# Kernel tuning notes

Measured on AMD Instinct MI355X. Metric: run time of the kernel, lower is better.

## Reference

```python
import jax, jax.numpy as jnp
import numpy as np

B, C, H, W, N = 256, 64, 36, 36, 2000
P = H * W  # 1296 mask pixels


def setup_inputs() -> dict:
    key = jax.random.key(0)
    k1, k2, k3 = jax.random.split(key, 3)
    x = jax.random.normal(k1, (B, C, H, W), dtype=jnp.float32)
    # init_scales rows 1 and 2 give (mean=0, std=0.01) for both param tensors
    mask_weights = 0.01 * jax.random.normal(k2, (P, C, N), dtype=jnp.float32)
    readout_weights = 0.01 * jax.random.normal(k3, (C, N), dtype=jnp.float32)
    return {"x": x, "mask_weights": mask_weights, "readout_weights": readout_weights}


def reference(x, mask_weights, readout_weights):
    # x: (B, C, H, W) -> flatten spatial dims to P
    b, c, h, w = x.shape
    x_flat = x.reshape(b, c, h * w)  # (B, C, P)
    # Per-channel spatial pooling fused with weighted channel sum:
    # masked[b,c,n] = sum_p x_flat[b,c,p] * mask_weights[p,c,n]
    # out[b,n]     = sum_c masked[b,c,n] * readout_weights[c,n]
    out = jnp.einsum("bcp,pcn,cn->bn", x_flat, mask_weights, readout_weights)
    # final_relu=False => no bias / softplus
    return out
```

## Files before the change

kernel.cpp:

```cpp
#include <hip/hip_runtime.h>

typedef unsigned short ushort_t;
typedef unsigned int uint_t;
typedef __attribute__((ext_vector_type(8))) short bf16x8;
typedef __attribute__((ext_vector_type(4))) float f32x4;

#define C_DIM 64
#define P_DIM 1296
#define N_DIM 2000
#define B_DIM 256
#define K_DIM (C_DIM * P_DIM)
#define XB_ELEMS (B_DIM * K_DIM)
#define XB_ELEMS_PAD (XB_ELEMS + 256)
#define XB_BYTES ((size_t)XB_ELEMS_PAD * 2)
#define SLICES 32
#define OUT_ELEMS (B_DIM * N_DIM)
#define NSTEP 82

static __device__ __forceinline__ ushort_t f2bf(float f) {
  unsigned u = __builtin_bit_cast(unsigned, f);
  u += 0x7fffu + ((u >> 16) & 1u);
  return (ushort_t)(u >> 16);
}

__global__ void klindt_cvt_kernel(const float4* __restrict__ x,
                                  unsigned long long* __restrict__ xb) {
  int idx = blockIdx.x * 256 + threadIdx.x;
  if (idx >= XB_ELEMS_PAD / 4) return;
  unsigned long long r = 0ull;
  if (idx < XB_ELEMS / 4) {
    float4 v = x[idx];
    r = (unsigned long long)f2bf(v.x) | ((unsigned long long)f2bf(v.y) << 16) |
        ((unsigned long long)f2bf(v.z) << 32) |
        ((unsigned long long)f2bf(v.w) << 48);
  }
  xb[idx] = r;
}

__global__ void __launch_bounds__(512, 4) klindt_gemm_kernel(
    const char* __restrict__ xbb, const char* __restrict__ mwb,
    const float* __restrict__ rw, float* __restrict__ partials) {
  __shared__ ushort_t sA[3][8192];

  const int tid = threadIdx.x;
  const int lane = tid & 63;
  const int wid = tid >> 6;
  const int r15 = lane & 15, g4 = lane >> 4;
  const int bid = blockIdx.x;
  const int slice = (bid & 7) + 8 * ((bid >> 3) & 3);
  const int n0 = (bid >> 5) * 128;
  const int c0 = slice * 2;

  f32x4 acc[16];
#pragma unroll
  for (int i = 0; i < 16; ++i) {
    acc[i][0] = 0.f; acc[i][1] = 0.f; acc[i][2] = 0.f; acc[i][3] = 0.f;
  }

  uint_t a_gbase[2]; int a_doff[2];
#pragma unroll
  for (int it = 0; it < 2; ++it) {
    int chunk = it * 512 + tid;
    int row = chunk >> 2, t4 = chunk & 3;
    int ss = t4 ^ ((row >> 1) & 3);
    a_gbase[it] = (uint_t)(row * K_DIM + ss * 8) * 2u;
    a_doff[it] = chunk * 8;
  }

  const int nidx = n0 + wid * 16 + r15;
  const bool okn = nidx < N_DIM;
  const uint_t nb4 = (uint_t)(okn ? nidx : (N_DIM - 1)) * 4u;
  const float rvl = okn ? rw[c0 * N_DIM + nidx] : 0.f;
  const float rvh = okn ? rw[(c0 + 1) * N_DIM + nidx] : 0.f;
  const uint_t pg = (uint_t)(g4 * 8);

  const int swz = g4 ^ ((r15 >> 1) & 3);
  const int aoffbase = r15 * 32 + swz * 8;

  float mv[8];
  bf16x8 bfr;

  auto issueA = [&](int buf, int t) {
    int half = (t >= 41) ? 1 : 0;
    int sp = t - 41 * half;
    uint_t kb = ((uint_t)(c0 + half) * (uint_t)P_DIM + (uint_t)sp * 32u) * 2u;
#pragma unroll
    for (int it = 0; it < 2; ++it) {
      const char* g = xbb + (a_gbase[it] + kb);
      __builtin_amdgcn_global_load_lds(
          (const __attribute__((address_space(1))) unsigned int*)g,
          (__attribute__((address_space(3))) unsigned int*)(&sA[buf][a_doff[it]]),
          16, 0, 0);
    }
  };
  auto issueB = [&](int t) {
    int half = (t >= 41) ? 1 : 0;
    int sp = t - 41 * half;
    uint_t p0 = (uint_t)sp * 32u + pg;
    if (p0 > 1288u) p0 = 1288u;
    const char* bp = mwb + (p0 * 512000u + (uint_t)(c0 + half) * 8000u + nb4);
#pragma unroll
    for (int j = 0; j < 8; ++j)
      mv[j] = *(const float*)(bp + (uint_t)j * 512000u);
  };
  auto cvtB = [&](int t) {
    float rv = (t >= 41) ? rvh : rvl;
    if ((t == 40 || t == 81) && g4 >= 2) rv = 0.f;
#pragma unroll
    for (int j = 0; j < 8; ++j) bfr[j] = (short)f2bf(mv[j] * rv);
  };
  auto computeStep = [&](int buf) {
    __builtin_amdgcn_s_setprio(1);
#pragma unroll
    for (int fm = 0; fm < 16; ++fm) {
      bf16x8 afr = *(const bf16x8*)(&sA[buf][aoffbase + fm * 512]);
      acc[fm] = __builtin_amdgcn_mfma_f32_16x16x32_bf16(afr, bfr, acc[fm],
                                                        0, 0, 0);
    }
    __builtin_amdgcn_s_setprio(0);
  };

  issueB(0);
  issueA(0, 0);
  issueA(1, 1);
  asm volatile("s_waitcnt vmcnt(2) lgkmcnt(0)" ::: "memory");
  __builtin_amdgcn_sched_barrier(0);
  __builtin_amdgcn_s_barrier();
  __builtin_amdgcn_sched_barrier(0);

  int cur = 0;
  for (int s = 0; s < 80; ++s) {
    int bufW = (cur >= 1) ? cur - 1 : 2;
    cvtB(s);
    issueB(s + 1);
    issueA(bufW, s + 2);
    computeStep(cur);
    asm volatile("s_waitcnt vmcnt(10) lgkmcnt(0)" ::: "memory");
    __builtin_amdgcn_sched_barrier(0);
    __builtin_amdgcn_s_barrier();
    __builtin_amdgcn_sched_barrier(0);
    cur = (cur == 2) ? 0 : cur + 1;
  }
  cvtB(80);
  issueB(81);
  computeStep(2);
  asm volatile("s_waitcnt vmcnt(8) lgkmcnt(0)" ::: "memory");
  __builtin_amdgcn_sched_barrier(0);
  __builtin_amdgcn_s_barrier();
  __builtin_amdgcn_sched_barrier(0);
  cvtB(81);
  computeStep(0);

  float* pb = partials + (size_t)slice * OUT_ELEMS;
  if (okn) {
#pragma unroll
    for (int fm = 0; fm < 16; ++fm) {
#pragma unroll
      for (int rr = 0; rr < 4; ++rr) {
        int m = fm * 16 + g4 * 4 + rr;
        pb[m * N_DIM + nidx] = acc[fm][rr];
      }
    }
  }
}

__global__ void klindt_reduce_kernel(const float* __restrict__ part,
                                     float* __restrict__ out) {
  int i = blockIdx.x * 256 + threadIdx.x;
  if (i < OUT_ELEMS) {
    float s = 0.f;
#pragma unroll
    for (int k = 0; k < SLICES; ++k) s += part[(size_t)k * OUT_ELEMS + i];
    out[i] = s;
  }
}

extern "C" void kernel_launch(void* const* d_in, const int* in_sizes, int n_in,
                              void* d_out, int out_size, void* d_ws,
                              size_t ws_size, hipStream_t stream) {
  (void)in_sizes; (void)n_in; (void)out_size; (void)ws_size;
  const float* x = (const float*)d_in[0];
  const char* mwb = (const char*)d_in[1];
  const float* rw = (const float*)d_in[2];
  float* out = (float*)d_out;

  char* xbb = (char*)d_ws;
  float* partials = (float*)((char*)d_ws + XB_BYTES);

  {
    int nvec = XB_ELEMS_PAD / 4;
    int grid = (nvec + 255) / 256;
    klindt_cvt_kernel<<<grid, 256, 0, stream>>>((const float4*)x,
                                                (unsigned long long*)xbb);
  }
  {
    klindt_gemm_kernel<<<512, 512, 0, stream>>>(xbb, mwb, rw, partials);
  }
  {
    int grid = (OUT_ELEMS + 255) / 256;
    klindt_reduce_kernel<<<grid, 256, 0, stream>>>(partials, out);
  }
}
```

Baseline: 247.9 us.

## Double K-step size to 64 with double-buffered LDS and ping-pong B registers

```diff
diff --git a/kernel.cpp b/kernel.cpp
--- a/kernel.cpp
+++ b/kernel.cpp
@@ -15,7 +15,7 @@
 #define XB_BYTES ((size_t)XB_ELEMS_PAD * 2)
 #define SLICES 32
 #define OUT_ELEMS (B_DIM * N_DIM)
-#define NSTEP 82
+#define NSTEP 42
 
 static __device__ __forceinline__ ushort_t f2bf(float f) {
   unsigned u = __builtin_bit_cast(unsigned, f);
@@ -40,7 +40,7 @@
 __global__ void __launch_bounds__(512, 4) klindt_gemm_kernel(
     const char* __restrict__ xbb, const char* __restrict__ mwb,
     const float* __restrict__ rw, float* __restrict__ partials) {
-  __shared__ ushort_t sA[3][8192];
+  __shared__ ushort_t sA[2][16384];
 
   const int tid = threadIdx.x;
   const int lane = tid & 63;
@@ -57,12 +57,12 @@
     acc[i][0] = 0.f; acc[i][1] = 0.f; acc[i][2] = 0.f; acc[i][3] = 0.f;
   }
 
-  uint_t a_gbase[2]; int a_doff[2];
-#pragma unroll
-  for (int it = 0; it < 2; ++it) {
+  uint_t a_gbase[4]; int a_doff[4];
+#pragma unroll
+  for (int it = 0; it < 4; ++it) {
     int chunk = it * 512 + tid;
-    int row = chunk >> 2, t4 = chunk & 3;
-    int ss = t4 ^ ((row >> 1) & 3);
+    int row = chunk >> 3, sl = chunk & 7;
+    int ss = sl ^ (row & 7);
     a_gbase[it] = (uint_t)(row * K_DIM + ss * 8) * 2u;
     a_doff[it] = chunk * 8;
   }
@@ -74,18 +74,18 @@
   const float rvh = okn ? rw[(c0 + 1) * N_DIM + nidx] : 0.f;
   const uint_t pg = (uint_t)(g4 * 8);
 
-  const int swz = g4 ^ ((r15 >> 1) & 3);
-  const int aoffbase = r15 * 32 + swz * 8;
-
-  float mv[8];
-  bf16x8 bfr;
+  const int swz7 = r15 & 7;
+  const int aoff0 = r15 * 128 + ((g4 ^ swz7) & 7) * 16;
+  const int aoff1 = r15 * 128 + (((g4 + 4) ^ swz7) & 7) * 16;
+
+  float mvE[16], mvO[16];
 
   auto issueA = [&](int buf, int t) {
-    int half = (t >= 41) ? 1 : 0;
-    int sp = t - 41 * half;
-    uint_t kb = ((uint_t)(c0 + half) * (uint_t)P_DIM + (uint_t)sp * 32u) * 2u;
-#pragma unroll
-    for (int it = 0; it < 2; ++it) {
+    int half = (t >= 21) ? 1 : 0;
+    int sp = t - 21 * half;
+    uint_t kb = ((uint_t)(c0 + half) * (uint_t)P_DIM + (uint_t)sp * 64u) * 2u;
+#pragma unroll
+    for (int it = 0; it < 4; ++it) {
       const char* g = xbb + (a_gbase[it] + kb);
       __builtin_amdgcn_global_load_lds(
           (const __attribute__((address_space(1))) unsigned int*)g,
@@ -93,63 +93,74 @@
           16, 0, 0);
     }
   };
-  auto issueB = [&](int t) {
-    int half = (t >= 41) ? 1 : 0;
-    int sp = t - 41 * half;
-    uint_t p0 = (uint_t)sp * 32u + pg;
-    if (p0 > 1288u) p0 = 1288u;
-    const char* bp = mwb + (p0 * 512000u + (uint_t)(c0 + half) * 8000u + nb4);
-#pragma unroll
-    for (int j = 0; j < 8; ++j)
-      mv[j] = *(const float*)(bp + (uint_t)j * 512000u);
-  };
-  auto cvtB = [&](int t) {
-    float rv = (t >= 41) ? rvh : rvl;
-    if ((t == 40 || t == 81) && g4 >= 2) rv = 0.f;
-#pragma unroll
-    for (int j = 0; j < 8; ++j) bfr[j] = (short)f2bf(mv[j] * rv);
-  };
-  auto computeStep = [&](int buf) {
-    __builtin_amdgcn_s_setprio(1);
-#pragma unroll
-    for (int fm = 0; fm < 16; ++fm) {
-      bf16x8 afr = *(const bf16x8*)(&sA[buf][aoffbase + fm * 512]);
-      acc[fm] = __builtin_amdgcn_mfma_f32_16x16x32_bf16(afr, bfr, acc[fm],
-                                                        0, 0, 0);
-    }
-    __builtin_amdgcn_s_setprio(0);
-  };
-
-  issueB(0);
+
+#define ISSUE_B(MV, T)                                                        \
+  do {                                                                        \
+    int half_ = ((T) >= 21) ? 1 : 0;                                          \
+    int sp_ = (T)-21 * half_;                                                 \
+    uint_t pa_ = (uint_t)(sp_ * 64) + pg;                                     \
+    uint_t pb_ = pa_ + 32u;                                                   \
+    if (pa_ > 1288u) pa_ = 1288u;       \
+    if (pb_ > 1288u) pb_ = 1288u;                                             \
+    uint_t cb_ = (uint_t)(c0 + half_) * 8000u + nb4;                          \
+    const char* ba_ = mwb + (pa_ * 512000u + cb_);                            \
+    const char* bb_ = mwb + (pb_ * 512000u + cb_);                            \
+    _Pragma("unroll") for (int j_ = 0; j_ < 8; ++j_)                          \
+        MV[j_] = *(const float*)(ba_ + (uint_t)j_ * 512000u);                 \
+    _Pragma("unroll") for (int j_ = 0; j_ < 8; ++j_)                          \
+        MV[8 + j_] = *(const float*)(bb_ + (uint_t)j_ * 512000u);             \
+  } while (0)
+
+#define CVT_COMPUTE(BUF, MV, T)                                               \
+  do {                                                                        \
+    int half_ = ((T) >= 21) ? 1 : 0;                                          \
+    int sp_ = (T)-21 * half_;                                                 \
+    float rv_ = half_ ? rvh : rvl;                                            \
+    float rva_ = (sp_ < 20 || g4 < 2) ? rv_ : 0.f;                            \
+    float rvb_ = (sp_ < 20) ? rv_ : 0.f;                                      \
+    bf16x8 b0_, b1_;                                                          \
+    _Pragma("unroll") for (int j_ = 0; j_ < 8; ++j_) {                        \
+      b0_[j_] = (short)f2bf(MV[j_] * rva_);                                   \
+      b1_[j_] = (short)f2bf(MV[8 + j_] * rvb_);                               \
+    }                                                                         \
+    __builtin_amdgcn_s_setprio(1);                                            \
+    _Pragma("unroll") for (int fm_ = 0; fm_ < 16; ++fm_) {                    \
+      bf16x8 a0_ = *(const bf16x8*)((const char*)&sA[BUF][0] +                \
+                                    (aoff0 + fm_ * 2048));                    \
+      acc[fm_] = __builtin_amdgcn_mfma_f32_16x16x32_bf16(a0_, b0_, acc[fm_],  \
+                                                         0, 0, 0);            \
+      bf16x8 a1_ = *(const bf16x8*)((const char*)&sA[BUF][0] +                \
+                                    (aoff1 + fm_ * 2048));                    \
+      acc[fm_] = __builtin_amdgcn_mfma_f32_16x16x32_bf16(a1_, b1_, acc[fm_],  \
+                                                         0, 0, 0);            \
+    }                                                                         \
+    __builtin_amdgcn_s_setprio(0);                                            \
+  } while (0)
+
   issueA(0, 0);
-  issueA(1, 1);
-  asm volatile("s_waitcnt vmcnt(2) lgkmcnt(0)" ::: "memory");
+  ISSUE_B(mvE, 0);
+  asm volatile("s_waitcnt vmcnt(16) lgkmcnt(0)" ::: "memory");
   __builtin_amdgcn_sched_barrier(0);
   __builtin_amdgcn_s_barrier();
   __builtin_amdgcn_sched_barrier(0);
 
-  int cur = 0;
-  for (int s = 0; s < 80; ++s) {
-    int bufW = (cur >= 1) ? cur - 1 : 2;
-    cvtB(s);
-    issueB(s + 1);
-    issueA(bufW, s + 2);
-    computeStep(cur);
-    asm volatile("s_waitcnt vmcnt(10) lgkmcnt(0)" ::: "memory");
-    __builtin_amdgcn_sched_barrier(0);
-    __builtin_amdgcn_s_barrier();
-    __builtin_amdgcn_sched_barrier(0);
-    cur = (cur == 2) ? 0 : cur + 1;
-  }
-  cvtB(80);
-  issueB(81);
-  computeStep(2);
-  asm volatile("s_waitcnt vmcnt(8) lgkmcnt(0)" ::: "memory");
-  __builtin_amdgcn_sched_barrier(0);
-  __builtin_amdgcn_s_barrier();
-  __builtin_amdgcn_sched_barrier(0);
-  cvtB(81);
-  computeStep(0);
+#define BODY(S, MV_CUR, MV_NEXT)                                              \
+  {                                                                           \
+    issueA(((S) + 1) & 1, (S) + 1);            \
+    ISSUE_B(MV_NEXT, (S) + 1);             \
+    CVT_COMPUTE((S)&1, MV_CUR, S);        \
+    asm volatile("s_waitcnt vmcnt(16) lgkmcnt(0)" ::: "memory");              \
+    __builtin_amdgcn_sched_barrier(0);                                        \
+    __builtin_amdgcn_s_barrier();                                             \
+    __builtin_amdgcn_sched_barrier(0);                                        \
+  }
+
+  for (int s = 0; s < 40; s += 2) {
+    BODY(s, mvE, mvO);
+    BODY(s + 1, mvO, mvE);
+  }
+  BODY(40, mvE, mvO);
+  CVT_COMPUTE(1, mvO, 41);
 
   float* pb = partials + (size_t)slice * OUT_ELEMS;
   if (okn) {
@@ -162,6 +173,9 @@
       }
     }
   }
+#undef BODY
+#undef ISSUE_B
+#undef CVT_COMPUTE
 }
 
 __global__ void klindt_reduce_kernel(const float* __restrict__ part,
```

New measurement: 244.8 us. No clear change (-1.2%).
